# Kernel tuning notes

Measured on AMD Instinct MI355X. Metric: run time of the kernel, lower is better.

Reference implementation:

```python
import jax, jax.numpy as jnp
import numpy as np

N_NODES = 100000
N_EDGES = 1600000
NUM_FEATURES = 256
HIDDEN_DIM = 128
NUM_CLASSES = 16


def setup_inputs() -> dict:
    key = jax.random.key(0)
    k1, k2, k3, k4 = jax.random.split(key, 4)
    x = jax.random.normal(k1, (N_NODES, NUM_FEATURES), dtype=jnp.float32)
    edge_index = jax.random.randint(k2, (2, N_EDGES), 0, N_NODES, dtype=jnp.int64)
    # Glorot-style init like PyG GCNConv's Linear
    W1 = jax.random.normal(k3, (NUM_FEATURES, HIDDEN_DIM), dtype=jnp.float32) / np.sqrt(NUM_FEATURES)
    b1 = jnp.zeros((HIDDEN_DIM,), dtype=jnp.float32)
    W2 = jax.random.normal(k4, (HIDDEN_DIM, NUM_CLASSES), dtype=jnp.float32) / np.sqrt(HIDDEN_DIM)
    b2 = jnp.zeros((NUM_CLASSES,), dtype=jnp.float32)
    return {"x": x, "edge_index": edge_index, "W1": W1, "b1": b1, "W2": W2, "b2": b2}


def _gcn_norm(edge_index, num_nodes):
    """PyG GCNConv default: add self-loops, symmetric deg^{-1/2} A deg^{-1/2} norm."""
    loops = jnp.arange(num_nodes, dtype=edge_index.dtype)
    row = jnp.concatenate([edge_index[0], loops])  # source
    col = jnp.concatenate([edge_index[1], loops])  # target
    deg = jax.ops.segment_sum(jnp.ones_like(col, dtype=jnp.float32), col,
                              num_segments=num_nodes)
    dinv = jnp.where(deg > 0, jax.lax.rsqrt(deg), 0.0)
    norm = dinv[row] * dinv[col]  # [E + N]
    return row, col, norm


def _gcn_conv(h, row, col, norm, num_nodes):
    # transform first (PyG: lin then propagate), then normalized sum-aggregate
    msg = h[row] * norm[:, None]            # [E+N, d] gather + scale
    return jax.ops.segment_sum(msg, col, num_segments=num_nodes)


def reference(x, edge_index, W1, b1, W2, b2):
    num_nodes = x.shape[0]
    row, col, norm = _gcn_norm(edge_index, num_nodes)
    h = x @ W1
    h = _gcn_conv(h, row, col, norm, num_nodes) + b1
    h = jax.nn.relu(h)
    h = h @ W2
    out = _gcn_conv(h, row, col, norm, num_nodes) + b2
    return out
```

## Files before the change

kernel.cpp:

```cpp
#include <hip/hip_runtime.h>

#define N_NODES 100000
#define N_EDGES 1600000
#define F_IN    256
#define F_HID   128
#define F_OUT   16

#define BSHIFT  9
#define BNODES  512
#define NB      196
#define ECAP    16384
#define CHUNK   4096
#define NCHUNK  ((N_EDGES + CHUNK - 1) / CHUNK)

typedef __attribute__((ext_vector_type(8))) short short8;
typedef __attribute__((ext_vector_type(4))) float float4v;

__device__ __forceinline__ unsigned int bf16_rn(float f) {
    unsigned int u = __float_as_uint(f);
    return (u + 0x7FFFu + ((u >> 16) & 1u)) >> 16;
}
__device__ __forceinline__ unsigned int pk2(float lo, float hi) {
    return bf16_rn(lo) | (bf16_rn(hi) << 16);
}
__device__ __forceinline__ float blo(unsigned int u) { return __uint_as_float(u << 16); }
__device__ __forceinline__ float bhi(unsigned int u) { return __uint_as_float(u & 0xFFFF0000u); }
__device__ __forceinline__ float bfu(unsigned short u) { return __uint_as_float(((unsigned int)u) << 16); }


__global__ __launch_bounds__(256) void k_binit(int* __restrict__ bcur) {
    int i = threadIdx.x;
    if (i < NB) bcur[i] = i * ECAP;
}

__global__ __launch_bounds__(256) void k_binscatter(const int* __restrict__ rowi,
                                                    const int* __restrict__ coli,
                                                    int* __restrict__ bcur,
                                                    unsigned int* __restrict__ ebuf) {
    __shared__ int cnt[NB], gbase[NB], run[NB];
    int tid = threadIdx.x;
    int e0 = blockIdx.x * CHUNK;
    for (int i = tid; i < NB; i += 256) { cnt[i] = 0; run[i] = 0; }
    __syncthreads();
    int d[16], s[16];
    #pragma unroll
    for (int i = 0; i < 16; i++) {
        int e = e0 + i * 256 + tid;
        if (e < N_EDGES) {
            d[i] = coli[e]; s[i] = rowi[e];
            atomicAdd(&cnt[d[i] >> BSHIFT], 1);
        } else d[i] = -1;
    }
    __syncthreads();
    for (int i = tid; i < NB; i += 256)
        gbase[i] = cnt[i] ? atomicAdd(&bcur[i], cnt[i]) : 0;
    __syncthreads();
    #pragma unroll
    for (int i = 0; i < 16; i++) {
        if (d[i] >= 0) {
            int b = d[i] >> BSHIFT;
            int off = atomicAdd(&run[b], 1);
            ebuf[gbase[b] + off] = ((unsigned int)(d[i] & 511) << 17) | (unsigned int)s[i];
        }
    }
}

__global__ __launch_bounds__(256) void k_finalize(const int* __restrict__ bcur,
                                                  const unsigned int* __restrict__ ebuf,
                                                  int* __restrict__ rp_start,
                                                  int* __restrict__ rp_end,
                                                  float* __restrict__ dinv,
                                                  int* __restrict__ esrc) {
    __shared__ int ndeg[BNODES];
    __shared__ int sc[BNODES];
    int tid = threadIdx.x;
    int b   = blockIdx.x;
    int nb0 = b << BSHIFT;
    int ebeg = b * ECAP, eend = bcur[b];
    ndeg[tid] = 0; ndeg[tid + 256] = 0;
    __syncthreads();
    for (int e = ebeg + tid; e < eend; e += 256)
        atomicAdd(&ndeg[ebuf[e] >> 17], 1);
    __syncthreads();
    int i0 = tid, i1 = tid + 256;
    sc[i0] = ndeg[i0]; sc[i1] = ndeg[i1];
    __syncthreads();
    for (int off = 1; off < BNODES; off <<= 1) {
        int v0 = (i0 >= off) ? sc[i0 - off] : 0;
        int v1 = (i1 >= off) ? sc[i1 - off] : 0;
        __syncthreads();
        sc[i0] += v0; sc[i1] += v1;
        __syncthreads();
    }
    #pragma unroll
    for (int k = 0; k < 2; k++) {
        int i = tid + k * 256;
        int n = nb0 + i;
        int deg = ndeg[i];
        int excl = sc[i] - deg;
        if (n < N_NODES) {
            rp_start[n] = ebeg + excl;
            rp_end[n]   = ebeg + excl + deg;
            dinv[n]     = rsqrtf(1.0f + (float)deg);
        }
        ndeg[i] = excl;
    }
    __syncthreads();
    for (int e = ebeg + tid; e < eend; e += 256) {
        unsigned int p = ebuf[e];
        int off = atomicAdd(&ndeg[p >> 17], 1);
        esrc[ebeg + off] = (int)(p & 0x1FFFFu);
    }
}


__global__ __launch_bounds__(256) void k_transW(const float* __restrict__ W1,
                                                ushort* __restrict__ Wt) {
    int t = blockIdx.x * 256 + threadIdx.x;
    int c = t & 127, k = t >> 7;
    Wt[c * 256 + k] = (ushort)bf16_rn(W1[k * 128 + c]);
}


__global__ __launch_bounds__(256) void k_gemm1(const float* __restrict__ x,
                                               const ushort* __restrict__ Wt,
                                               const float* __restrict__ dinv,
                                               ushort* __restrict__ g1) {
    __shared__ ushort Bl[128 * 256];
    const int tid = threadIdx.x;
    const int w = tid >> 6;
    const int l = tid & 63;
    const int m = l & 15;
    const int q = l >> 4;
    const int R0 = blockIdx.x * 128;

    {
        const uint4* Wg = (const uint4*)Wt;
        uint4* Bl4 = (uint4*)Bl;
        #pragma unroll
        for (int it = 0; it < 16; it++) {
            int i = it * 256 + tid;
            int c = i >> 5, j = i & 31;
            Bl4[c * 32 + (j ^ (c & 7))] = Wg[i];
        }
    }
    __syncthreads();

    int r0 = R0 + w * 32 + m;      if (r0 > N_NODES - 1) r0 = N_NODES - 1;
    int r1 = R0 + w * 32 + 16 + m; if (r1 > N_NODES - 1) r1 = N_NODES - 1;
    const float* xr0 = &x[(size_t)r0 * F_IN + q * 8];
    const float* xr1 = &x[(size_t)r1 * F_IN + q * 8];
    const short8* Bl8 = (const short8*)Bl;

    float4v acc[2][8];
    #pragma unroll
    for (int i = 0; i < 2; i++)
        #pragma unroll
        for (int j = 0; j < 8; j++) acc[i][j] = (float4v){0.f, 0.f, 0.f, 0.f};

    #pragma unroll 2
    for (int kt = 0; kt < F_IN; kt += 32) {
        float4 a0 = *(const float4*)&xr0[kt];
        float4 a1 = *(const float4*)&xr0[kt + 4];
        float4 b0 = *(const float4*)&xr1[kt];
        float4 b1 = *(const float4*)&xr1[kt + 4];
        short8 af0, af1;
        ((uint*)&af0)[0] = pk2(a0.x, a0.y); ((uint*)&af0)[1] = pk2(a0.z, a0.w);
        ((uint*)&af0)[2] = pk2(a1.x, a1.y); ((uint*)&af0)[3] = pk2(a1.z, a1.w);
        ((uint*)&af1)[0] = pk2(b0.x, b0.y); ((uint*)&af1)[1] = pk2(b0.z, b0.w);
        ((uint*)&af1)[2] = pk2(b1.x, b1.y); ((uint*)&af1)[3] = pk2(b1.z, b1.w);
        int jq = (kt >> 3) + q;
        #pragma unroll
        for (int n = 0; n < 8; n++) {
            int col = n * 16 + m;
            short8 bfr = Bl8[col * 32 + (jq ^ (col & 7))];
            acc[0][n] = __builtin_amdgcn_mfma_f32_16x16x32_bf16(af0, bfr, acc[0][n], 0, 0, 0);
            acc[1][n] = __builtin_amdgcn_mfma_f32_16x16x32_bf16(af1, bfr, acc[1][n], 0, 0, 0);
        }
    }

    const int rbase = R0 + w * 32 + q * 4;
    float dv0[4], dv1[4];
    #pragma unroll
    for (int r = 0; r < 4; r++) {
        int v0 = rbase + r;      dv0[r] = (v0 < N_NODES) ? dinv[v0] : 0.f;
        int v1 = rbase + 16 + r; dv1[r] = (v1 < N_NODES) ? dinv[v1] : 0.f;
    }
    #pragma unroll
    for (int n = 0; n < 8; n++) {
        #pragma unroll
        for (int r = 0; r < 4; r++) {
            int v0 = rbase + r;
            if (v0 < N_NODES)
                g1[v0 * F_HID + n * 16 + m] = (ushort)bf16_rn(dv0[r] * acc[0][n][r]);
            int v1 = rbase + 16 + r;
            if (v1 < N_NODES)
                g1[v1 * F_HID + n * 16 + m] = (ushort)bf16_rn(dv1[r] * acc[1][n][r]);
        }
    }
}


__global__ __launch_bounds__(256) void k_agg1g2(const int* __restrict__ rp_start,
                                                const int* __restrict__ rp_end,
                                                const int* __restrict__ esrc,
                                                const float* __restrict__ dinv,
                                                const unsigned int* __restrict__ g1,
                                                const float* __restrict__ b1,
                                                const float* __restrict__ W2,
                                                ushort* __restrict__ g2b) {
    __shared__ float hl[4][132];
    const int tid  = threadIdx.x;
    const int wave = tid >> 6;
    const int lane = tid & 63;
    const int col  = lane & 15, part = lane >> 4;

    float w2r[32];
    #pragma unroll
    for (int i = 0; i < 32; i++) w2r[i] = W2[i * 64 + lane];

    float2 bb = ((const float2*)b1)[lane];

    #pragma unroll 1
    for (int j = 0; j < 4; j++) {
        const int node = blockIdx.x * 16 + j * 4 + wave;
        int s = rp_start[node], t = rp_end[node];
        unsigned int u = g1[node * 64 + lane];
        float ax = blo(u), ay = bhi(u);
        int e = s;
        for (; e + 7 < t; e += 8) {
            int r0 = esrc[e],     r1 = esrc[e + 1], r2 = esrc[e + 2], r3 = esrc[e + 3];
            int r4 = esrc[e + 4], r5 = esrc[e + 5], r6 = esrc[e + 6], r7 = esrc[e + 7];
            unsigned int u0 = g1[r0 * 64 + lane], u1 = g1[r1 * 64 + lane];
            unsigned int u2 = g1[r2 * 64 + lane], u3 = g1[r3 * 64 + lane];
            unsigned int u4 = g1[r4 * 64 + lane], u5 = g1[r5 * 64 + lane];
            unsigned int u6 = g1[r6 * 64 + lane], u7 = g1[r7 * 64 + lane];
            ax += blo(u0) + blo(u1) + blo(u2) + blo(u3)
                + blo(u4) + blo(u5) + blo(u6) + blo(u7);
            ay += bhi(u0) + bhi(u1) + bhi(u2) + bhi(u3)
                + bhi(u4) + bhi(u5) + bhi(u6) + bhi(u7);
        }
        for (; e + 3 < t; e += 4) {
            int r0 = esrc[e], r1 = esrc[e + 1], r2 = esrc[e + 2], r3 = esrc[e + 3];
            unsigned int u0 = g1[r0 * 64 + lane], u1 = g1[r1 * 64 + lane];
            unsigned int u2 = g1[r2 * 64 + lane], u3 = g1[r3 * 64 + lane];
            ax += blo(u0) + blo(u1) + blo(u2) + blo(u3);
            ay += bhi(u0) + bhi(u1) + bhi(u2) + bhi(u3);
        }
        for (; e < t; e++) {
            unsigned int u0 = g1[esrc[e] * 64 + lane];
            ax += blo(u0); ay += bhi(u0);
        }
        float wv = dinv[node];
        hl[wave][lane * 2]     = fmaxf(fmaf(wv, ax, bb.x), 0.0f);
        hl[wave][lane * 2 + 1] = fmaxf(fmaf(wv, ay, bb.y), 0.0f);

        float acc = 0.f;
        #pragma unroll
        for (int i = 0; i < 32; i++)
            acc = fmaf(hl[wave][i * 4 + part], w2r[i], acc);
        acc += __shfl_xor(acc, 16);
        acc += __shfl_xor(acc, 32);
        if (lane < 16) g2b[node * 16 + col] = (ushort)bf16_rn(wv * acc);
    }
}


__global__ __launch_bounds__(256) void k_agg2(const int* __restrict__ rp_start,
                                              const int* __restrict__ rp_end,
                                              const int* __restrict__ esrc,
                                              const float* __restrict__ dinv,
                                              const ushort* __restrict__ g2b,
                                              const float* __restrict__ b2,
                                              float* __restrict__ out) {
    int gid = blockIdx.x * 256 + threadIdx.x;
    int node = gid >> 4;
    int f = gid & 15;
    if (node >= N_NODES) return;
    int s = rp_start[node], t = rp_end[node];
    float acc = bfu(g2b[node * 16 + f]);
    int e = s;
    for (; e + 7 < t; e += 8) {
        float a0 = bfu(g2b[esrc[e] * 16 + f]),     a1 = bfu(g2b[esrc[e + 1] * 16 + f]);
        float a2 = bfu(g2b[esrc[e + 2] * 16 + f]), a3 = bfu(g2b[esrc[e + 3] * 16 + f]);
        float a4 = bfu(g2b[esrc[e + 4] * 16 + f]), a5 = bfu(g2b[esrc[e + 5] * 16 + f]);
        float a6 = bfu(g2b[esrc[e + 6] * 16 + f]), a7 = bfu(g2b[esrc[e + 7] * 16 + f]);
        acc += a0 + a1 + a2 + a3 + a4 + a5 + a6 + a7;
    }
    for (; e + 3 < t; e += 4) {
        acc += bfu(g2b[esrc[e] * 16 + f]) + bfu(g2b[esrc[e + 1] * 16 + f])
             + bfu(g2b[esrc[e + 2] * 16 + f]) + bfu(g2b[esrc[e + 3] * 16 + f]);
    }
    for (; e < t; e++) acc += bfu(g2b[esrc[e] * 16 + f]);
    out[node * 16 + f] = fmaf(dinv[node], acc, b2[f]);
}


extern "C" void kernel_launch(void* const* d_in, const int* in_sizes, int n_in,
                              void* d_out, int out_size, void* d_ws, size_t ws_size,
                              hipStream_t stream) {
    const float* x   = (const float*)d_in[0];
    const int*   ei  = (const int*)d_in[1];
    const float* W1  = (const float*)d_in[2];
    const float* b1  = (const float*)d_in[3];
    const float* W2  = (const float*)d_in[4];
    const float* b2  = (const float*)d_in[5];
    float* out = (float*)d_out;

    const int* rowi = ei;
    const int* coli = ei + N_EDGES;

    char* ws = (char*)d_ws;
    int*          bcur     = (int*)(ws + 0);
    int*          rp_start = (int*)(ws + 8192);
    int*          rp_end   = (int*)(ws + 524288);
    float*        dinv     = (float*)(ws + 1048576);
    unsigned int* ebuf     = (unsigned int*)(ws + 2097152);
    int*          esrc     = (int*)(ws + 16777216);
    ushort*       Wt       = (ushort*)(ws + 31457280);
    ushort*       g1       = (ushort*)(ws + 33554432);
    ushort*       g2b      = (ushort*)(ws + 62914560);

    k_binit     <<<1, 256, 0, stream>>>(bcur);
    k_binscatter<<<NCHUNK, 256, 0, stream>>>(rowi, coli, bcur, ebuf);
    k_finalize  <<<NB, 256, 0, stream>>>(bcur, ebuf, rp_start, rp_end, dinv, esrc);
    k_transW    <<<128, 256, 0, stream>>>(W1, Wt);

    k_gemm1     <<<(N_NODES + 127) / 128, 256, 0, stream>>>(x, Wt, dinv, g1);
    k_agg1g2    <<<N_NODES / 16, 256, 0, stream>>>(rp_start, rp_end, esrc, dinv,
                                                   (const unsigned int*)g1, b1, W2, g2b);
    k_agg2      <<<(N_NODES * 16 + 255) / 256, 256, 0, stream>>>(rp_start, rp_end, esrc,
                                                                 dinv, g2b, b2, out);
}
```

Before: 328.3 us.

## Split layer-1 aggregation into feature slices and move W2 GEMV to separate kernel

The hidden features are now stored as eight column slices of 16 bf16 values each, and the first aggregation runs one slice per block. Each slice of 3.2MB is meant to stay cache-resident while it is gathered randomly, instead of gathering full 256-byte rows from a 25MB table. The fused W2 projection moves into a new kernel that reads an fp32 hidden buffer written by the aggregation. In exchange the edge index lists are read eight times over, there is an extra kernel launch, and the fp32 intermediate adds about 51MB of writes and reads.

```diff
diff --git a/kernel.cpp b/kernel.cpp
--- a/kernel.cpp
+++ b/kernel.cpp
@@ -13,8 +13,13 @@
 #define CHUNK   4096
 #define NCHUNK  ((N_EDGES + CHUNK - 1) / CHUNK)
 
+#define NSLICE      8
+#define SLICE_WORDS (N_NODES * 8)
+#define AGG1_NB     782
+
 typedef __attribute__((ext_vector_type(8))) short short8;
 typedef __attribute__((ext_vector_type(4))) float float4v;
+typedef __attribute__((ext_vector_type(2))) float float2v;
 
 __device__ __forceinline__ unsigned int bf16_rn(float f) {
     unsigned int u = __float_as_uint(f);
@@ -188,80 +193,128 @@
     }
     #pragma unroll
     for (int n = 0; n < 8; n++) {
+        ushort* gs = g1 + (size_t)n * (N_NODES * 16);
         #pragma unroll
         for (int r = 0; r < 4; r++) {
             int v0 = rbase + r;
             if (v0 < N_NODES)
-                g1[v0 * F_HID + n * 16 + m] = (ushort)bf16_rn(dv0[r] * acc[0][n][r]);
+                gs[v0 * 16 + m] = (ushort)bf16_rn(dv0[r] * acc[0][n][r]);
             int v1 = rbase + 16 + r;
             if (v1 < N_NODES)
-                g1[v1 * F_HID + n * 16 + m] = (ushort)bf16_rn(dv1[r] * acc[1][n][r]);
-        }
-    }
-}
-
-
-__global__ __launch_bounds__(256) void k_agg1g2(const int* __restrict__ rp_start,
-                                                const int* __restrict__ rp_end,
-                                                const int* __restrict__ esrc,
-                                                const float* __restrict__ dinv,
-                                                const unsigned int* __restrict__ g1,
-                                                const float* __restrict__ b1,
-                                                const float* __restrict__ W2,
-                                                ushort* __restrict__ g2b) {
-    __shared__ float hl[4][132];
+                gs[v1 * 16 + m] = (ushort)bf16_rn(dv1[r] * acc[1][n][r]);
+        }
+    }
+}
+
+
+__global__ __launch_bounds__(256) void k_agg1(const int* __restrict__ rp_start,
+                                              const int* __restrict__ rp_end,
+                                              const int* __restrict__ esrc,
+                                              const float* __restrict__ dinv,
+                                              const ushort* __restrict__ g1,
+                                              const float* __restrict__ b1,
+                                              float* __restrict__ hpart) {
+    const int tid  = threadIdx.x;
+    const int wave = tid >> 6;
+    const int lane = tid & 63;
+    const int ns   = lane >> 3;
+    const int fp   = lane & 7;
+    const int s    = blockIdx.x & 7;
+    const int nb   = blockIdx.x >> 3;
+    const unsigned int* gs = (const unsigned int*)g1 + (size_t)s * SLICE_WORDS;
+    const float2 bb = ((const float2*)(b1 + s * 16))[fp];
+
+    #pragma unroll 1
+    for (int j = 0; j < 4; j++) {
+        const int node  = nb * 128 + wave * 32 + j * 8 + ns;
+        const bool valid = node < N_NODES;
+        const int nc = valid ? node : (N_NODES - 1);
+        int e = __builtin_nontemporal_load(rp_start + nc);
+        int t = valid ? __builtin_nontemporal_load(rp_end + nc) : e;
+        unsigned int u = gs[nc * 8 + fp];
+        float ax = blo(u), ay = bhi(u);
+        for (; e + 7 < t; e += 8) {
+            int r0 = __builtin_nontemporal_load(esrc + e);
+            int r1 = __builtin_nontemporal_load(esrc + e + 1);
+            int r2 = __builtin_nontemporal_load(esrc + e + 2);
+            int r3 = __builtin_nontemporal_load(esrc + e + 3);
+            int r4 = __builtin_nontemporal_load(esrc + e + 4);
+            int r5 = __builtin_nontemporal_load(esrc + e + 5);
+            int r6 = __builtin_nontemporal_load(esrc + e + 6);
+            int r7 = __builtin_nontemporal_load(esrc + e + 7);
+            unsigned int u0 = gs[r0 * 8 + fp], u1 = gs[r1 * 8 + fp];
+            unsigned int u2 = gs[r2 * 8 + fp], u3 = gs[r3 * 8 + fp];
+            unsigned int u4 = gs[r4 * 8 + fp], u5 = gs[r5 * 8 + fp];
+            unsigned int u6 = gs[r6 * 8 + fp], u7 = gs[r7 * 8 + fp];
+            ax += blo(u0) + blo(u1) + blo(u2) + blo(u3)
+                + blo(u4) + blo(u5) + blo(u6) + blo(u7);
+            ay += bhi(u0) + bhi(u1) + bhi(u2) + bhi(u3)
+                + bhi(u4) + bhi(u5) + bhi(u6) + bhi(u7);
+        }
+        for (; e + 3 < t; e += 4) {
+            int r0 = __builtin_nontemporal_load(esrc + e);
+            int r1 = __builtin_nontemporal_load(esrc + e + 1);
+            int r2 = __builtin_nontemporal_load(esrc + e + 2);
+            int r3 = __builtin_nontemporal_load(esrc + e + 3);
+            unsigned int u0 = gs[r0 * 8 + fp], u1 = gs[r1 * 8 + fp];
+            unsigned int u2 = gs[r2 * 8 + fp], u3 = gs[r3 * 8 + fp];
+            ax += blo(u0) + blo(u1) + blo(u2) + blo(u3);
+            ay += bhi(u0) + bhi(u1) + bhi(u2) + bhi(u3);
+        }
+        for (; e < t; e++) {
+            int r0 = __builtin_nontemporal_load(esrc + e);
+            unsigned int u0 = gs[r0 * 8 + fp];
+            ax += blo(u0); ay += bhi(u0);
+        }
+        if (valid) {
+            float wv = __builtin_nontemporal_load(dinv + nc);
+            float2v h;
+            h.x = fmaxf(fmaf(wv, ax, bb.x), 0.0f);
+            h.y = fmaxf(fmaf(wv, ay, bb.y), 0.0f);
+            __builtin_nontemporal_store(h,
+                (float2v*)&hpart[(size_t)node * F_HID + s * 16 + 2 * fp]);
+        }
+    }
+}
+
+
+__global__ __launch_bounds__(256) void k_g2(const float* __restrict__ hpart,
+                                            const float* __restrict__ dinv,
+                                            const float* __restrict__ W2,
+                                            ushort* __restrict__ g2b) {
+    __shared__ float hl[16 * 128];
     const int tid  = threadIdx.x;
     const int wave = tid >> 6;
     const int lane = tid & 63;
     const int col  = lane & 15, part = lane >> 4;
+    const int n0   = blockIdx.x * 16;
 
     float w2r[32];
     #pragma unroll
     for (int i = 0; i < 32; i++) w2r[i] = W2[i * 64 + lane];
 
-    float2 bb = ((const float2*)b1)[lane];
+    {
+        const float4v* src = (const float4v*)(hpart + (size_t)n0 * F_HID);
+        float4v* dst = (float4v*)hl;
+        dst[tid]       = src[tid];
+        dst[tid + 256] = src[tid + 256];
+    }
+    __syncthreads();
 
     #pragma unroll 1
     for (int j = 0; j < 4; j++) {
-        const int node = blockIdx.x * 16 + j * 4 + wave;
-        int s = rp_start[node], t = rp_end[node];
-        unsigned int u = g1[node * 64 + lane];
-        float ax = blo(u), ay = bhi(u);
-        int e = s;
-        for (; e + 7 < t; e += 8) {
-            int r0 = esrc[e],     r1 = esrc[e + 1], r2 = esrc[e + 2], r3 = esrc[e + 3];
-            int r4 = esrc[e + 4], r5 = esrc[e + 5], r6 = esrc[e + 6], r7 = esrc[e + 7];
-            unsigned int u0 = g1[r0 * 64 + lane], u1 = g1[r1 * 64 + lane];
-            unsigned int u2 = g1[r2 * 64 + lane], u3 = g1[r3 * 64 + lane];
-            unsigned int u4 = g1[r4 * 64 + lane], u5 = g1[r5 * 64 + lane];
-            unsigned int u6 = g1[r6 * 64 + lane], u7 = g1[r7 * 64 + lane];
-            ax += blo(u0) + blo(u1) + blo(u2) + blo(u3)
-                + blo(u4) + blo(u5) + blo(u6) + blo(u7);
-            ay += bhi(u0) + bhi(u1) + bhi(u2) + bhi(u3)
-                + bhi(u4) + bhi(u5) + bhi(u6) + bhi(u7);
-        }
-        for (; e + 3 < t; e += 4) {
-            int r0 = esrc[e], r1 = esrc[e + 1], r2 = esrc[e + 2], r3 = esrc[e + 3];
-            unsigned int u0 = g1[r0 * 64 + lane], u1 = g1[r1 * 64 + lane];
-            unsigned int u2 = g1[r2 * 64 + lane], u3 = g1[r3 * 64 + lane];
-            ax += blo(u0) + blo(u1) + blo(u2) + blo(u3);
-            ay += bhi(u0) + bhi(u1) + bhi(u2) + bhi(u3);
-        }
-        for (; e < t; e++) {
-            unsigned int u0 = g1[esrc[e] * 64 + lane];
-            ax += blo(u0); ay += bhi(u0);
-        }
-        float wv = dinv[node];
-        hl[wave][lane * 2]     = fmaxf(fmaf(wv, ax, bb.x), 0.0f);
-        hl[wave][lane * 2 + 1] = fmaxf(fmaf(wv, ay, bb.y), 0.0f);
-
+        const int nl   = wave * 4 + j;
+        const int node = n0 + nl;
         float acc = 0.f;
         #pragma unroll
         for (int i = 0; i < 32; i++)
-            acc = fmaf(hl[wave][i * 4 + part], w2r[i], acc);
+            acc = fmaf(hl[nl * 128 + i * 4 + part], w2r[i], acc);
         acc += __shfl_xor(acc, 16);
         acc += __shfl_xor(acc, 32);
-        if (lane < 16) g2b[node * 16 + col] = (ushort)bf16_rn(wv * acc);
+        if (lane < 16) {
+            float wv = dinv[node];
+            g2b[node * 16 + col] = (ushort)bf16_rn(wv * acc);
+        }
     }
 }
 
@@ -320,6 +373,7 @@
     ushort*       Wt       = (ushort*)(ws + 31457280);
     ushort*       g1       = (ushort*)(ws + 33554432);
     ushort*       g2b      = (ushort*)(ws + 62914560);
+    float*        hpart    = (float*)(ws + 67108864);
 
     k_binit     <<<1, 256, 0, stream>>>(bcur);
     k_binscatter<<<NCHUNK, 256, 0, stream>>>(rowi, coli, bcur, ebuf);
@@ -327,8 +381,9 @@
     k_transW    <<<128, 256, 0, stream>>>(W1, Wt);
 
     k_gemm1     <<<(N_NODES + 127) / 128, 256, 0, stream>>>(x, Wt, dinv, g1);
-    k_agg1g2    <<<N_NODES / 16, 256, 0, stream>>>(rp_start, rp_end, esrc, dinv,
-                                                   (const unsigned int*)g1, b1, W2, g2b);
+    k_agg1      <<<NSLICE * AGG1_NB, 256, 0, stream>>>(rp_start, rp_end, esrc, dinv,
+                                                       g1, b1, hpart);
+    k_g2        <<<N_NODES / 16, 256, 0, stream>>>(hpart, dinv, W2, g2b);
     k_agg2      <<<(N_NODES * 16 + 255) / 256, 256, 0, stream>>>(rp_start, rp_end, esrc,
                                                                  dinv, g2b, b2, out);
 }
```

Result: slower. 455.0 us (+38.6%).
